# Optimization experiments

Hardware: AMD Instinct MI355X
Metric: run time of the kernel (lower is better)

Reference implementation:

```python
import jax, jax.numpy as jnp
import numpy as np

N_NODES = 100000
DIM = 4
N_EDGES = 3200000


def setup_inputs() -> dict:
    key = jax.random.key(0)
    k1, k2, k3 = jax.random.split(key, 3)
    x = jax.random.normal(k1, (N_NODES, DIM), dtype=jnp.float32)
    edge_index = jax.random.randint(k2, (2, N_EDGES), 0, N_NODES, dtype=jnp.int64)
    boo_values = jax.random.normal(k3, (N_EDGES, DIM, DIM), dtype=jnp.float32)
    return {"x": x, "edge_index": edge_index, "boo_values": boo_values}


def _spmv(x, edge_index, A):
    # y_i = sum_j A_{ij} x_j ; edge e = (row=edge_index[0], col=edge_index[1])
    # PyG flow='target_to_source': gather x at col, scatter-add at row.
    row, col = edge_index[0], edge_index[1]
    msg = jnp.einsum('eij,ej->ei', A, x[col])  # [E, dim]
    return jax.ops.segment_sum(msg, row, num_segments=x.shape[0])


def _spmv_t(x, edge_index, A):
    # y_j = sum_i A_{ij}^T x_i ; flow='source_to_target': gather at row, scatter at col.
    row, col = edge_index[0], edge_index[1]
    msg = jnp.einsum('eji,ej->ei', A, x[row])  # A^T matvec, [E, dim]
    return jax.ops.segment_sum(msg, col, num_segments=x.shape[0])


def reference(x, edge_index, boo_values):
    lt_x = _spmv_t(x, edge_index, boo_values)   # L^T x
    return _spmv(lt_x, edge_index, boo_values)  # L (L^T x)
```

## Files before the change

### kernel.cpp

```cpp
#include <hip/hip_runtime.h>

static constexpr int N_NODES = 100000;
static constexpr int N_EDGES = 3200000;
static constexpr int SHIFT  = 8;
static constexpr int NPB    = 1 << SHIFT;
static constexpr int NBK    = (N_NODES + NPB - 1) / NPB;
static constexpr int WGC    = 1024;
static constexpr int CHUNK  = N_EDGES / WGC;


__global__ void __launch_bounds__(256) k_count(
    const int* __restrict__ row, const int* __restrict__ col,
    unsigned* __restrict__ cmC, unsigned* __restrict__ cmR)
{
    __shared__ unsigned hC[NBK], hR[NBK];
    for (int b = threadIdx.x; b < NBK; b += 256) { hC[b] = 0u; hR[b] = 0u; }
    __syncthreads();
    int w = blockIdx.x, e0 = w * CHUNK;
    for (int e = e0 + threadIdx.x; e < e0 + CHUNK; e += 256) {
        atomicAdd(&hC[col[e] >> SHIFT], 1u);
        atomicAdd(&hR[row[e] >> SHIFT], 1u);
    }
    __syncthreads();
    for (int b = threadIdx.x; b < NBK; b += 256) {
        cmC[(size_t)b * WGC + w] = hC[b];
        cmR[(size_t)b * WGC + w] = hR[b];
    }
}

__global__ void __launch_bounds__(256) k_prefix(
    unsigned* __restrict__ cmC, unsigned* __restrict__ cmR,
    unsigned* __restrict__ totC, unsigned* __restrict__ totR)
{
    int warp = (blockIdx.x * 256 + threadIdx.x) >> 6;
    int lane = threadIdx.x & 63;
    if (warp >= 2 * NBK) return;
    unsigned* cm  = (warp < NBK) ? cmC : cmR;
    unsigned* tot = (warp < NBK) ? totC : totR;
    int b = (warp < NBK) ? warp : warp - NBK;
    unsigned* rowp = cm + (size_t)b * WGC;
    unsigned carry = 0;
    for (int base = 0; base < WGC; base += 64) {
        unsigned v = rowp[base + lane];
        unsigned inc = v;
        for (int off = 1; off < 64; off <<= 1) {
            unsigned t = __shfl_up(inc, off, 64);
            if (lane >= off) inc += t;
        }
        rowp[base + lane] = carry + inc - v;
        carry += __shfl(inc, 63, 64);
    }
    if (lane == 0) tot[b] = carry;
}

__global__ void __launch_bounds__(256) k_scan(
    const unsigned* __restrict__ totC, const unsigned* __restrict__ totR,
    unsigned* __restrict__ baseC, unsigned* __restrict__ baseR)
{
    const unsigned* tot = blockIdx.x ? totR : totC;
    unsigned* base = blockIdx.x ? baseR : baseC;
    __shared__ unsigned tsum[256];
    int tid = threadIdx.x;
    unsigned a0 = (2 * tid     < NBK) ? tot[2 * tid]     : 0u;
    unsigned a1 = (2 * tid + 1 < NBK) ? tot[2 * tid + 1] : 0u;
    tsum[tid] = a0 + a1;
    __syncthreads();
    for (int off = 1; off < 256; off <<= 1) {
        unsigned v = (tid >= off) ? tsum[tid - off] : 0u;
        __syncthreads();
        tsum[tid] += v;
        __syncthreads();
    }
    unsigned ex = tid ? tsum[tid - 1] : 0u;
    if (2 * tid     < NBK) base[2 * tid]     = ex;
    if (2 * tid + 1 < NBK) base[2 * tid + 1] = ex + a0;
}

__global__ void __launch_bounds__(256) k_partition(
    const int* __restrict__ key,
    const int* __restrict__ pay,
    const unsigned* __restrict__ cm,
    const unsigned* __restrict__ base,
    uint2* __restrict__ perm)
{
    __shared__ unsigned hist[NBK];
    __shared__ unsigned runstart[NBK + 1];
    __shared__ unsigned gdst[NBK];
    __shared__ unsigned tsum[256];
    __shared__ uint2 stage[CHUNK];
    int w = blockIdx.x, tid = threadIdx.x, e0 = w * CHUNK;

    for (int b = tid; b < NBK; b += 256) {
        hist[b] = 0u;
        gdst[b] = base[b] + cm[(size_t)b * WGC + w];
    }
    __syncthreads();
    for (int e = e0 + tid; e < e0 + CHUNK; e += 256)
        atomicAdd(&hist[key[e] >> SHIFT], 1u);
    __syncthreads();
    unsigned a0 = (2 * tid     < NBK) ? hist[2 * tid]     : 0u;
    unsigned a1 = (2 * tid + 1 < NBK) ? hist[2 * tid + 1] : 0u;
    tsum[tid] = a0 + a1;
    __syncthreads();
    for (int off = 1; off < 256; off <<= 1) {
        unsigned v = (tid >= off) ? tsum[tid - off] : 0u;
        __syncthreads();
        tsum[tid] += v;
        __syncthreads();
    }
    unsigned ex = tid ? tsum[tid - 1] : 0u;
    if (2 * tid     <= NBK) runstart[2 * tid]     = ex;
    if (2 * tid + 1 <= NBK) runstart[2 * tid + 1] = ex + a0;
    __syncthreads();
    for (int b = tid; b < NBK; b += 256) hist[b] = runstart[b];
    __syncthreads();
    for (int e = e0 + tid; e < e0 + CHUNK; e += 256) {
        int k = key[e], p = pay[e];
        int b = k >> SHIFT;
        unsigned pos = atomicAdd(&hist[b], 1u);
        stage[pos] = make_uint2((unsigned)e,
                                (unsigned)p | ((unsigned)(k & (NPB - 1)) << 17));
    }
    __syncthreads();
    for (int s = tid; s < CHUNK; s += 256) {
        int lo = 0, hi = NBK;
        while (hi - lo > 1) {
            int mid = (lo + hi) >> 1;
            if (runstart[mid] <= (unsigned)s) lo = mid; else hi = mid;
        }
        perm[(size_t)gdst[lo] + (unsigned)s - runstart[lo]] = stage[s];
    }
}

template<int TRANS>
__global__ void __launch_bounds__(512) k_reduce(
    const uint2* __restrict__ perm,
    const float4* __restrict__ vin,
    const float4* __restrict__ boo,
    const unsigned* __restrict__ base, const unsigned* __restrict__ tot,
    float4* __restrict__ vout)
{
    __shared__ float acc[4][NPB];
    int b = blockIdx.x, tid = threadIdx.x;
    for (int i = tid; i < 4 * NPB; i += 512) ((float*)acc)[i] = 0.f;
    __syncthreads();
    unsigned start = base[b], n = tot[b];
    for (unsigned i = start + tid; i < start + n; i += 512) {
        uint2 rec = perm[i];
        unsigned e   = rec.x;
        unsigned src = rec.y & 0x1FFFFu;
        unsigned loc = rec.y >> 17;
        float4 v  = vin[src];
        float4 a0 = boo[(size_t)e * 4 + 0];
        float4 a1 = boo[(size_t)e * 4 + 1];
        float4 a2 = boo[(size_t)e * 4 + 2];
        float4 a3 = boo[(size_t)e * 4 + 3];
        float m0, m1, m2, m3;
        if (TRANS) {
            m0 = a0.x * v.x + a1.x * v.y + a2.x * v.z + a3.x * v.w;
            m1 = a0.y * v.x + a1.y * v.y + a2.y * v.z + a3.y * v.w;
            m2 = a0.z * v.x + a1.z * v.y + a2.z * v.z + a3.z * v.w;
            m3 = a0.w * v.x + a1.w * v.y + a2.w * v.z + a3.w * v.w;
        } else {
            m0 = a0.x * v.x + a0.y * v.y + a0.z * v.z + a0.w * v.w;
            m1 = a1.x * v.x + a1.y * v.y + a1.z * v.z + a1.w * v.w;
            m2 = a2.x * v.x + a2.y * v.y + a2.z * v.z + a2.w * v.w;
            m3 = a3.x * v.x + a3.y * v.y + a3.z * v.z + a3.w * v.w;
        }
        atomicAdd(&acc[0][loc], m0);
        atomicAdd(&acc[1][loc], m1);
        atomicAdd(&acc[2][loc], m2);
        atomicAdd(&acc[3][loc], m3);
    }
    __syncthreads();
    for (int i = tid; i < NPB; i += 512) {
        int node = b * NPB + i;
        if (node < N_NODES)
            vout[node] = make_float4(acc[0][i], acc[1][i], acc[2][i], acc[3][i]);
    }
}


__global__ void __launch_bounds__(256) llt_pass1(
    const float* __restrict__ x, const int* __restrict__ row_idx,
    const int* __restrict__ col_idx, const float* __restrict__ boo,
    float* __restrict__ lt)
{
    int t = blockIdx.x * blockDim.x + threadIdx.x;
    if (t >= N_EDGES * 4) return;
    int e = t >> 2, i = t & 3;
    int r = row_idx[e], c = col_idx[e];
    const float* A = boo + (size_t)e * 16;
    const float* xv = x + (size_t)r * 4;
    float m = A[0*4+i]*xv[0] + A[1*4+i]*xv[1] + A[2*4+i]*xv[2] + A[3*4+i]*xv[3];
    atomicAdd(lt + (size_t)c * 4 + i, m);
}

__global__ void __launch_bounds__(256) llt_pass2(
    const float4* __restrict__ lt, const int* __restrict__ row_idx,
    const int* __restrict__ col_idx, const float4* __restrict__ boo,
    float* __restrict__ out)
{
    int t = blockIdx.x * blockDim.x + threadIdx.x;
    if (t >= N_EDGES * 4) return;
    int e = t >> 2, i = t & 3;
    int r = row_idx[e], c = col_idx[e];
    float4 arow = boo[(size_t)e * 4 + i];
    float4 lv = lt[c];
    float m = arow.x*lv.x + arow.y*lv.y + arow.z*lv.z + arow.w*lv.w;
    atomicAdd(out + (size_t)r * 4 + i, m);
}


extern "C" void kernel_launch(void* const* d_in, const int* in_sizes, int n_in,
                              void* d_out, int out_size, void* d_ws, size_t ws_size,
                              hipStream_t stream) {
    const float4* x = (const float4*)d_in[0];
    const int* edge_index = (const int*)d_in[1];
    const float4* boo = (const float4*)d_in[2];
    const int* row = edge_index;
    const int* col = edge_index + N_EDGES;
    float4* out = (float4*)d_out;

    auto align256 = [](size_t v) { return (v + 255) & ~(size_t)255; };
    const size_t sz_cm   = align256((size_t)NBK * WGC * 4);
    const size_t sz_vec  = align256((size_t)NBK * 4);
    const size_t sz_perm = align256((size_t)N_EDGES * 8);
    const size_t sz_lt   = align256((size_t)NBK * NPB * 16);
    const size_t need = 2 * sz_cm + 4 * sz_vec + sz_perm + sz_lt;

    if (ws_size >= need) {
        char* p = (char*)d_ws;
        unsigned* cmC   = (unsigned*)p; p += sz_cm;
        unsigned* cmR   = (unsigned*)p; p += sz_cm;
        unsigned* totC  = (unsigned*)p; p += sz_vec;
        unsigned* totR  = (unsigned*)p; p += sz_vec;
        unsigned* baseC = (unsigned*)p; p += sz_vec;
        unsigned* baseR = (unsigned*)p; p += sz_vec;
        uint2*    perm  = (uint2*)p;    p += sz_perm;
        float4*   lt    = (float4*)p;   p += sz_lt;

        k_count<<<WGC, 256, 0, stream>>>(row, col, cmC, cmR);
        k_prefix<<<(2 * NBK + 3) / 4, 256, 0, stream>>>(cmC, cmR, totC, totR);
        k_scan<<<2, 256, 0, stream>>>(totC, totR, baseC, baseR);
        k_partition<<<WGC, 256, 0, stream>>>(col, row, cmC, baseC, perm);
        k_reduce<1><<<NBK, 512, 0, stream>>>(perm, x, boo, baseC, totC, lt);
        k_partition<<<WGC, 256, 0, stream>>>(row, col, cmR, baseR, perm);
        k_reduce<0><<<NBK, 512, 0, stream>>>(perm, (const float4*)lt, boo, baseR, totR, out);
    } else {
        float* ltf = (float*)d_ws;
        hipMemsetAsync(ltf, 0, (size_t)N_NODES * 4 * sizeof(float), stream);
        hipMemsetAsync(out, 0, (size_t)N_NODES * 4 * sizeof(float), stream);
        const int grid = (N_EDGES * 4 + 255) / 256;
        llt_pass1<<<grid, 256, 0, stream>>>((const float*)x, row, col, (const float*)boo, ltf);
        llt_pass2<<<grid, 256, 0, stream>>>((const float4*)ltf, row, col, boo, (float*)out);
    }
}
```

Measured before the change: 265.4 us.

## Compute messages in partition pass, scatter bf16-packed messages with byte tags

The per-edge 4x4 matvec moves from the reduce kernel into the partition kernel. There the boo values are read in edge order (coalesced) rather than through a permuted gather. The resulting message is packed into four bf16 values (8 bytes) plus a one-byte local-node tag and scattered into bucket order, so the reduce kernel only streams messages and does LDS atomics. The work-group count also rises from 1024 to 1280. Rounding messages to bf16 adds precision loss in both passes, which could exceed tolerance.

```diff
diff --git a/kernel.cpp b/kernel.cpp
--- a/kernel.cpp
+++ b/kernel.cpp
@@ -5,9 +5,17 @@
 static constexpr int SHIFT  = 8;
 static constexpr int NPB    = 1 << SHIFT;
 static constexpr int NBK    = (N_NODES + NPB - 1) / NPB;
-static constexpr int WGC    = 1024;
+static constexpr int WGC    = 1280;
 static constexpr int CHUNK  = N_EDGES / WGC;
 
+__device__ __forceinline__ unsigned bf16rne(float f) {
+    unsigned u = __float_as_uint(f);
+    u += 0x7fffu + ((u >> 16) & 1u);
+    return u >> 16;
+}
+__device__ __forceinline__ unsigned pack2(float lo, float hi) {
+    return bf16rne(lo) | (bf16rne(hi) << 16);
+}
 
 __global__ void __launch_bounds__(256) k_count(
     const int* __restrict__ row, const int* __restrict__ col,
@@ -76,18 +84,23 @@
     if (2 * tid + 1 < NBK) base[2 * tid + 1] = ex + a0;
 }
 
-__global__ void __launch_bounds__(256) k_partition(
+template<int TRANS>
+__global__ void __launch_bounds__(256) k_partition_msg(
     const int* __restrict__ key,
     const int* __restrict__ pay,
+    const float4* __restrict__ vin,
+    const float4* __restrict__ boo,
     const unsigned* __restrict__ cm,
     const unsigned* __restrict__ base,
-    uint2* __restrict__ perm)
-{
+    uint2* __restrict__ msgbuf, unsigned char* __restrict__ tagbuf)
+{
+    __shared__ int      karr[CHUNK];
+    __shared__ uint2    smsg[CHUNK];
+    __shared__ unsigned char stag[CHUNK];
     __shared__ unsigned hist[NBK];
     __shared__ unsigned runstart[NBK + 1];
     __shared__ unsigned gdst[NBK];
     __shared__ unsigned tsum[256];
-    __shared__ uint2 stage[CHUNK];
     int w = blockIdx.x, tid = threadIdx.x, e0 = w * CHUNK;
 
     for (int b = tid; b < NBK; b += 256) {
@@ -95,8 +108,11 @@
         gdst[b] = base[b] + cm[(size_t)b * WGC + w];
     }
     __syncthreads();
-    for (int e = e0 + tid; e < e0 + CHUNK; e += 256)
-        atomicAdd(&hist[key[e] >> SHIFT], 1u);
+    for (int l = tid; l < CHUNK; l += 256) {
+        int k = key[e0 + l];
+        karr[l] = k;
+        atomicAdd(&hist[k >> SHIFT], 1u);
+    }
     __syncthreads();
     unsigned a0 = (2 * tid     < NBK) ? hist[2 * tid]     : 0u;
     unsigned a1 = (2 * tid + 1 < NBK) ? hist[2 * tid + 1] : 0u;
@@ -114,29 +130,49 @@
     __syncthreads();
     for (int b = tid; b < NBK; b += 256) hist[b] = runstart[b];
     __syncthreads();
-    for (int e = e0 + tid; e < e0 + CHUNK; e += 256) {
-        int k = key[e], p = pay[e];
+
+    for (int l = tid; l < CHUNK; l += 256) {
+        int e = e0 + l;
+        int k = karr[l];
+        int p = pay[e];
         int b = k >> SHIFT;
+        float4 v  = vin[p];
+        float4 q0 = boo[(size_t)e * 4 + 0];
+        float4 q1 = boo[(size_t)e * 4 + 1];
+        float4 q2 = boo[(size_t)e * 4 + 2];
+        float4 q3 = boo[(size_t)e * 4 + 3];
+        float m0, m1, m2, m3;
+        if (TRANS) {
+            m0 = q0.x * v.x + q1.x * v.y + q2.x * v.z + q3.x * v.w;
+            m1 = q0.y * v.x + q1.y * v.y + q2.y * v.z + q3.y * v.w;
+            m2 = q0.z * v.x + q1.z * v.y + q2.z * v.z + q3.z * v.w;
+            m3 = q0.w * v.x + q1.w * v.y + q2.w * v.z + q3.w * v.w;
+        } else {
+            m0 = q0.x * v.x + q0.y * v.y + q0.z * v.z + q0.w * v.w;
+            m1 = q1.x * v.x + q1.y * v.y + q1.z * v.z + q1.w * v.w;
+            m2 = q2.x * v.x + q2.y * v.y + q2.z * v.z + q2.w * v.w;
+            m3 = q3.x * v.x + q3.y * v.y + q3.z * v.z + q3.w * v.w;
+        }
         unsigned pos = atomicAdd(&hist[b], 1u);
-        stage[pos] = make_uint2((unsigned)e,
-                                (unsigned)p | ((unsigned)(k & (NPB - 1)) << 17));
-    }
-    __syncthreads();
+        smsg[pos] = make_uint2(pack2(m0, m1), pack2(m2, m3));
+        stag[pos] = (unsigned char)(k & (NPB - 1));
+    }
+    __syncthreads();
+
     for (int s = tid; s < CHUNK; s += 256) {
         int lo = 0, hi = NBK;
         while (hi - lo > 1) {
             int mid = (lo + hi) >> 1;
             if (runstart[mid] <= (unsigned)s) lo = mid; else hi = mid;
         }
-        perm[(size_t)gdst[lo] + (unsigned)s - runstart[lo]] = stage[s];
-    }
-}
-
-template<int TRANS>
-__global__ void __launch_bounds__(512) k_reduce(
-    const uint2* __restrict__ perm,
-    const float4* __restrict__ vin,
-    const float4* __restrict__ boo,
+        size_t g = (size_t)gdst[lo] + (unsigned)s - runstart[lo];
+        msgbuf[g] = smsg[s];
+        tagbuf[g] = stag[s];
+    }
+}
+
+__global__ void __launch_bounds__(512) k_reduce_msg(
+    const uint2* __restrict__ msgbuf, const unsigned char* __restrict__ tagbuf,
     const unsigned* __restrict__ base, const unsigned* __restrict__ tot,
     float4* __restrict__ vout)
 {
@@ -146,31 +182,12 @@
     __syncthreads();
     unsigned start = base[b], n = tot[b];
     for (unsigned i = start + tid; i < start + n; i += 512) {
-        uint2 rec = perm[i];
-        unsigned e   = rec.x;
-        unsigned src = rec.y & 0x1FFFFu;
-        unsigned loc = rec.y >> 17;
-        float4 v  = vin[src];
-        float4 a0 = boo[(size_t)e * 4 + 0];
-        float4 a1 = boo[(size_t)e * 4 + 1];
-        float4 a2 = boo[(size_t)e * 4 + 2];
-        float4 a3 = boo[(size_t)e * 4 + 3];
-        float m0, m1, m2, m3;
-        if (TRANS) {
-            m0 = a0.x * v.x + a1.x * v.y + a2.x * v.z + a3.x * v.w;
-            m1 = a0.y * v.x + a1.y * v.y + a2.y * v.z + a3.y * v.w;
-            m2 = a0.z * v.x + a1.z * v.y + a2.z * v.z + a3.z * v.w;
-            m3 = a0.w * v.x + a1.w * v.y + a2.w * v.z + a3.w * v.w;
-        } else {
-            m0 = a0.x * v.x + a0.y * v.y + a0.z * v.z + a0.w * v.w;
-            m1 = a1.x * v.x + a1.y * v.y + a1.z * v.z + a1.w * v.w;
-            m2 = a2.x * v.x + a2.y * v.y + a2.z * v.z + a2.w * v.w;
-            m3 = a3.x * v.x + a3.y * v.y + a3.z * v.z + a3.w * v.w;
-        }
-        atomicAdd(&acc[0][loc], m0);
-        atomicAdd(&acc[1][loc], m1);
-        atomicAdd(&acc[2][loc], m2);
-        atomicAdd(&acc[3][loc], m3);
+        uint2 m = msgbuf[i];
+        int loc = tagbuf[i];
+        atomicAdd(&acc[0][loc], __uint_as_float(m.x << 16));
+        atomicAdd(&acc[1][loc], __uint_as_float(m.x & 0xffff0000u));
+        atomicAdd(&acc[2][loc], __uint_as_float(m.y << 16));
+        atomicAdd(&acc[3][loc], __uint_as_float(m.y & 0xffff0000u));
     }
     __syncthreads();
     for (int i = tid; i < NPB; i += 512) {
@@ -225,9 +242,10 @@
     auto align256 = [](size_t v) { return (v + 255) & ~(size_t)255; };
     const size_t sz_cm   = align256((size_t)NBK * WGC * 4);
     const size_t sz_vec  = align256((size_t)NBK * 4);
-    const size_t sz_perm = align256((size_t)N_EDGES * 8);
+    const size_t sz_msg  = align256((size_t)N_EDGES * 8);
+    const size_t sz_tag  = align256((size_t)N_EDGES);
     const size_t sz_lt   = align256((size_t)NBK * NPB * 16);
-    const size_t need = 2 * sz_cm + 4 * sz_vec + sz_perm + sz_lt;
+    const size_t need = 2 * sz_cm + 4 * sz_vec + sz_msg + sz_tag + sz_lt;
 
     if (ws_size >= need) {
         char* p = (char*)d_ws;
@@ -237,16 +255,17 @@
         unsigned* totR  = (unsigned*)p; p += sz_vec;
         unsigned* baseC = (unsigned*)p; p += sz_vec;
         unsigned* baseR = (unsigned*)p; p += sz_vec;
-        uint2*    perm  = (uint2*)p;    p += sz_perm;
+        uint2*    msg   = (uint2*)p;    p += sz_msg;
+        unsigned char* tag = (unsigned char*)p; p += sz_tag;
         float4*   lt    = (float4*)p;   p += sz_lt;
 
         k_count<<<WGC, 256, 0, stream>>>(row, col, cmC, cmR);
         k_prefix<<<(2 * NBK + 3) / 4, 256, 0, stream>>>(cmC, cmR, totC, totR);
         k_scan<<<2, 256, 0, stream>>>(totC, totR, baseC, baseR);
-        k_partition<<<WGC, 256, 0, stream>>>(col, row, cmC, baseC, perm);
-        k_reduce<1><<<NBK, 512, 0, stream>>>(perm, x, boo, baseC, totC, lt);
-        k_partition<<<WGC, 256, 0, stream>>>(row, col, cmR, baseR, perm);
-        k_reduce<0><<<NBK, 512, 0, stream>>>(perm, (const float4*)lt, boo, baseR, totR, out);
+        k_partition_msg<1><<<WGC, 256, 0, stream>>>(col, row, x, boo, cmC, baseC, msg, tag);
+        k_reduce_msg<<<NBK, 512, 0, stream>>>(msg, tag, baseC, totC, lt);
+        k_partition_msg<0><<<WGC, 256, 0, stream>>>(row, col, (const float4*)lt, boo, cmR, baseR, msg, tag);
+        k_reduce_msg<<<NBK, 512, 0, stream>>>(msg, tag, baseR, totR, out);
     } else {
         float* ltf = (float*)d_ws;
         hipMemsetAsync(ltf, 0, (size_t)N_NODES * 4 * sizeof(float), stream);
```

Result: slower. 398.4 us (+50.1%).

## Split reduce blocks four ways with lane-per-row edge processing and merge pass

Applied to the files above, without the earlier changes.

Each bucket's reduce is now split across four workgroups, with the partial sums written to separate buffers and combined by a new merge kernel. Inside the reduce, four lanes share one edge and each loads one row of the 4x4 block, which gives coalesced 64-byte loads. The transposed case reduces its products across those lanes with shuffles. The aim is more parallelism (391 blocks become 1564) and better memory coalescing, at the cost of extra partial-buffer traffic, two extra launches, and redundant loads of perm and vin per lane.

```diff
diff --git a/kernel.cpp b/kernel.cpp
--- a/kernel.cpp
+++ b/kernel.cpp
@@ -5,8 +5,10 @@
 static constexpr int SHIFT  = 8;
 static constexpr int NPB    = 1 << SHIFT;
 static constexpr int NBK    = (N_NODES + NPB - 1) / NPB;
+static constexpr int SLOTS  = NBK * NPB;
 static constexpr int WGC    = 1024;
 static constexpr int CHUNK  = N_EDGES / WGC;
+static constexpr int PSPLIT = 4;
 
 
 __global__ void __launch_bounds__(256) k_count(
@@ -138,46 +140,55 @@
     const float4* __restrict__ vin,
     const float4* __restrict__ boo,
     const unsigned* __restrict__ base, const unsigned* __restrict__ tot,
-    float4* __restrict__ vout)
-{
-    __shared__ float acc[4][NPB];
-    int b = blockIdx.x, tid = threadIdx.x;
-    for (int i = tid; i < 4 * NPB; i += 512) ((float*)acc)[i] = 0.f;
+    float4* __restrict__ part)
+{
+    __shared__ float acc[NPB][4];
+    int b = blockIdx.x / PSPLIT, sub = blockIdx.x % PSPLIT;
+    int tid = threadIdx.x;
+    for (int i = tid; i < NPB * 4; i += 512) ((float*)acc)[i] = 0.f;
     __syncthreads();
     unsigned start = base[b], n = tot[b];
-    for (unsigned i = start + tid; i < start + n; i += 512) {
+    int g = tid >> 2;
+    int q = tid & 3;
+    for (unsigned i = start + sub * 128 + g; i < start + n; i += 128 * PSPLIT) {
         uint2 rec = perm[i];
         unsigned e   = rec.x;
         unsigned src = rec.y & 0x1FFFFu;
         unsigned loc = rec.y >> 17;
         float4 v  = vin[src];
-        float4 a0 = boo[(size_t)e * 4 + 0];
-        float4 a1 = boo[(size_t)e * 4 + 1];
-        float4 a2 = boo[(size_t)e * 4 + 2];
-        float4 a3 = boo[(size_t)e * 4 + 3];
-        float m0, m1, m2, m3;
+        float4 ch = boo[(size_t)e * 4 + q];
+        float mq;
         if (TRANS) {
-            m0 = a0.x * v.x + a1.x * v.y + a2.x * v.z + a3.x * v.w;
-            m1 = a0.y * v.x + a1.y * v.y + a2.y * v.z + a3.y * v.w;
-            m2 = a0.z * v.x + a1.z * v.y + a2.z * v.z + a3.z * v.w;
-            m3 = a0.w * v.x + a1.w * v.y + a2.w * v.z + a3.w * v.w;
+            float vq = (q == 0) ? v.x : (q == 1) ? v.y : (q == 2) ? v.z : v.w;
+            float p0 = vq * ch.x, p1 = vq * ch.y, p2 = vq * ch.z, p3 = vq * ch.w;
+            p0 += __shfl_xor(p0, 1); p1 += __shfl_xor(p1, 1);
+            p2 += __shfl_xor(p2, 1); p3 += __shfl_xor(p3, 1);
+            p0 += __shfl_xor(p0, 2); p1 += __shfl_xor(p1, 2);
+            p2 += __shfl_xor(p2, 2); p3 += __shfl_xor(p3, 2);
+            mq = (q == 0) ? p0 : (q == 1) ? p1 : (q == 2) ? p2 : p3;
         } else {
-            m0 = a0.x * v.x + a0.y * v.y + a0.z * v.z + a0.w * v.w;
-            m1 = a1.x * v.x + a1.y * v.y + a1.z * v.z + a1.w * v.w;
-            m2 = a2.x * v.x + a2.y * v.y + a2.z * v.z + a2.w * v.w;
-            m3 = a3.x * v.x + a3.y * v.y + a3.z * v.z + a3.w * v.w;
+            mq = ch.x * v.x + ch.y * v.y + ch.z * v.z + ch.w * v.w;
         }
-        atomicAdd(&acc[0][loc], m0);
-        atomicAdd(&acc[1][loc], m1);
-        atomicAdd(&acc[2][loc], m2);
-        atomicAdd(&acc[3][loc], m3);
+        atomicAdd(&acc[loc][q], mq);
     }
     __syncthreads();
     for (int i = tid; i < NPB; i += 512) {
-        int node = b * NPB + i;
-        if (node < N_NODES)
-            vout[node] = make_float4(acc[0][i], acc[1][i], acc[2][i], acc[3][i]);
-    }
+        part[(size_t)sub * SLOTS + (size_t)b * NPB + i] =
+            make_float4(acc[i][0], acc[i][1], acc[i][2], acc[i][3]);
+    }
+}
+
+__global__ void __launch_bounds__(256) k_merge(
+    const float4* __restrict__ part, float4* __restrict__ vout)
+{
+    int s = blockIdx.x * 256 + threadIdx.x;
+    if (s >= N_NODES) return;
+    float4 r = part[s];
+    for (int sub = 1; sub < PSPLIT; ++sub) {
+        float4 t = part[(size_t)sub * SLOTS + s];
+        r.x += t.x; r.y += t.y; r.z += t.z; r.w += t.w;
+    }
+    vout[s] = r;
 }
 
 
@@ -226,8 +237,9 @@
     const size_t sz_cm   = align256((size_t)NBK * WGC * 4);
     const size_t sz_vec  = align256((size_t)NBK * 4);
     const size_t sz_perm = align256((size_t)N_EDGES * 8);
-    const size_t sz_lt   = align256((size_t)NBK * NPB * 16);
-    const size_t need = 2 * sz_cm + 4 * sz_vec + sz_perm + sz_lt;
+    const size_t sz_lt   = align256((size_t)SLOTS * 16);
+    const size_t sz_part = align256((size_t)PSPLIT * SLOTS * 16);
+    const size_t need = 2 * sz_cm + 4 * sz_vec + sz_perm + sz_lt + sz_part;
 
     if (ws_size >= need) {
         char* p = (char*)d_ws;
@@ -239,14 +251,17 @@
         unsigned* baseR = (unsigned*)p; p += sz_vec;
         uint2*    perm  = (uint2*)p;    p += sz_perm;
         float4*   lt    = (float4*)p;   p += sz_lt;
+        float4*   part  = (float4*)p;   p += sz_part;
 
         k_count<<<WGC, 256, 0, stream>>>(row, col, cmC, cmR);
         k_prefix<<<(2 * NBK + 3) / 4, 256, 0, stream>>>(cmC, cmR, totC, totR);
         k_scan<<<2, 256, 0, stream>>>(totC, totR, baseC, baseR);
         k_partition<<<WGC, 256, 0, stream>>>(col, row, cmC, baseC, perm);
-        k_reduce<1><<<NBK, 512, 0, stream>>>(perm, x, boo, baseC, totC, lt);
+        k_reduce<1><<<NBK * PSPLIT, 512, 0, stream>>>(perm, x, boo, baseC, totC, part);
+        k_merge<<<(N_NODES + 255) / 256, 256, 0, stream>>>(part, lt);
         k_partition<<<WGC, 256, 0, stream>>>(row, col, cmR, baseR, perm);
-        k_reduce<0><<<NBK, 512, 0, stream>>>(perm, (const float4*)lt, boo, baseR, totR, out);
+        k_reduce<0><<<NBK * PSPLIT, 512, 0, stream>>>(perm, (const float4*)lt, boo, baseR, totR, part);
+        k_merge<<<(N_NODES + 255) / 256, 256, 0, stream>>>(part, out);
     } else {
         float* ltf = (float*)d_ws;
         hipMemsetAsync(ltf, 0, (size_t)N_NODES * 4 * sizeof(float), stream);
```

Result: no change. 262.5 us (-1.1%).

## Use coarse node buckets with split reduction blocks and partial-sum merge

Applied to the files above, without the earlier changes.

Replaces the 391 power-of-two node buckets with 26 buckets of 3848 nodes each. This cuts per-block histogram, scan and counter-matrix work in the count, prefix and partition kernels, and the shared scans become serial loops. Each bucket's reduction is split across 20 workgroups, each writing a private partial-sum slice, and a new merge kernel sums the 20 slices. The cost is extra global traffic for partial buffers, two more launches, and more shared memory per reduce block, which may lower occupancy.

```diff
diff --git a/kernel.cpp b/kernel.cpp
--- a/kernel.cpp
+++ b/kernel.cpp
@@ -2,11 +2,12 @@
 
 static constexpr int N_NODES = 100000;
 static constexpr int N_EDGES = 3200000;
-static constexpr int SHIFT  = 8;
-static constexpr int NPB    = 1 << SHIFT;
-static constexpr int NBK    = (N_NODES + NPB - 1) / NPB;
+static constexpr int NBK    = 26;
+static constexpr int NPB    = 3848;
+static constexpr int SLOTS  = NBK * NPB;
 static constexpr int WGC    = 1024;
 static constexpr int CHUNK  = N_EDGES / WGC;
+static constexpr int PSPLIT = 20;
 
 
 __global__ void __launch_bounds__(256) k_count(
@@ -14,17 +15,17 @@
     unsigned* __restrict__ cmC, unsigned* __restrict__ cmR)
 {
     __shared__ unsigned hC[NBK], hR[NBK];
-    for (int b = threadIdx.x; b < NBK; b += 256) { hC[b] = 0u; hR[b] = 0u; }
+    if (threadIdx.x < NBK) { hC[threadIdx.x] = 0u; hR[threadIdx.x] = 0u; }
     __syncthreads();
     int w = blockIdx.x, e0 = w * CHUNK;
     for (int e = e0 + threadIdx.x; e < e0 + CHUNK; e += 256) {
-        atomicAdd(&hC[col[e] >> SHIFT], 1u);
-        atomicAdd(&hR[row[e] >> SHIFT], 1u);
-    }
-    __syncthreads();
-    for (int b = threadIdx.x; b < NBK; b += 256) {
-        cmC[(size_t)b * WGC + w] = hC[b];
-        cmR[(size_t)b * WGC + w] = hR[b];
+        atomicAdd(&hC[col[e] / NPB], 1u);
+        atomicAdd(&hR[row[e] / NPB], 1u);
+    }
+    __syncthreads();
+    if (threadIdx.x < NBK) {
+        cmC[(size_t)threadIdx.x * WGC + w] = hC[threadIdx.x];
+        cmR[(size_t)threadIdx.x * WGC + w] = hR[threadIdx.x];
     }
 }
 
@@ -53,73 +54,55 @@
     if (lane == 0) tot[b] = carry;
 }
 
-__global__ void __launch_bounds__(256) k_scan(
+__global__ void __launch_bounds__(64) k_scan(
     const unsigned* __restrict__ totC, const unsigned* __restrict__ totR,
     unsigned* __restrict__ baseC, unsigned* __restrict__ baseR)
 {
-    const unsigned* tot = blockIdx.x ? totR : totC;
-    unsigned* base = blockIdx.x ? baseR : baseC;
-    __shared__ unsigned tsum[256];
-    int tid = threadIdx.x;
-    unsigned a0 = (2 * tid     < NBK) ? tot[2 * tid]     : 0u;
-    unsigned a1 = (2 * tid + 1 < NBK) ? tot[2 * tid + 1] : 0u;
-    tsum[tid] = a0 + a1;
-    __syncthreads();
-    for (int off = 1; off < 256; off <<= 1) {
-        unsigned v = (tid >= off) ? tsum[tid - off] : 0u;
-        __syncthreads();
-        tsum[tid] += v;
-        __syncthreads();
-    }
-    unsigned ex = tid ? tsum[tid - 1] : 0u;
-    if (2 * tid     < NBK) base[2 * tid]     = ex;
-    if (2 * tid + 1 < NBK) base[2 * tid + 1] = ex + a0;
-}
-
-__global__ void __launch_bounds__(256) k_partition(
+    if (threadIdx.x == 0) {
+        unsigned s = 0;
+        for (int b = 0; b < NBK; ++b) { baseC[b] = s; s += totC[b]; }
+    } else if (threadIdx.x == 1) {
+        unsigned s = 0;
+        for (int b = 0; b < NBK; ++b) { baseR[b] = s; s += totR[b]; }
+    }
+}
+
+__global__ void __launch_bounds__(256) k_part(
     const int* __restrict__ key,
     const int* __restrict__ pay,
     const unsigned* __restrict__ cm,
     const unsigned* __restrict__ base,
     uint2* __restrict__ perm)
 {
+    __shared__ uint2 stage[CHUNK];
     __shared__ unsigned hist[NBK];
     __shared__ unsigned runstart[NBK + 1];
     __shared__ unsigned gdst[NBK];
-    __shared__ unsigned tsum[256];
-    __shared__ uint2 stage[CHUNK];
     int w = blockIdx.x, tid = threadIdx.x, e0 = w * CHUNK;
 
-    for (int b = tid; b < NBK; b += 256) {
-        hist[b] = 0u;
-        gdst[b] = base[b] + cm[(size_t)b * WGC + w];
+    if (tid < NBK) {
+        hist[tid] = 0u;
+        gdst[tid] = base[tid] + cm[(size_t)tid * WGC + w];
     }
     __syncthreads();
     for (int e = e0 + tid; e < e0 + CHUNK; e += 256)
-        atomicAdd(&hist[key[e] >> SHIFT], 1u);
-    __syncthreads();
-    unsigned a0 = (2 * tid     < NBK) ? hist[2 * tid]     : 0u;
-    unsigned a1 = (2 * tid + 1 < NBK) ? hist[2 * tid + 1] : 0u;
-    tsum[tid] = a0 + a1;
-    __syncthreads();
-    for (int off = 1; off < 256; off <<= 1) {
-        unsigned v = (tid >= off) ? tsum[tid - off] : 0u;
-        __syncthreads();
-        tsum[tid] += v;
-        __syncthreads();
-    }
-    unsigned ex = tid ? tsum[tid - 1] : 0u;
-    if (2 * tid     <= NBK) runstart[2 * tid]     = ex;
-    if (2 * tid + 1 <= NBK) runstart[2 * tid + 1] = ex + a0;
-    __syncthreads();
-    for (int b = tid; b < NBK; b += 256) hist[b] = runstart[b];
+        atomicAdd(&hist[key[e] / NPB], 1u);
+    __syncthreads();
+    if (tid == 0) {
+        unsigned s = 0;
+        for (int b = 0; b < NBK; ++b) { runstart[b] = s; s += hist[b]; }
+        runstart[NBK] = s;
+    }
+    __syncthreads();
+    if (tid < NBK) hist[tid] = runstart[tid];
     __syncthreads();
     for (int e = e0 + tid; e < e0 + CHUNK; e += 256) {
         int k = key[e], p = pay[e];
-        int b = k >> SHIFT;
+        int b = k / NPB;
+        int loc = k - b * NPB;
         unsigned pos = atomicAdd(&hist[b], 1u);
         stage[pos] = make_uint2((unsigned)e,
-                                (unsigned)p | ((unsigned)(k & (NPB - 1)) << 17));
+                                (unsigned)p | ((unsigned)loc << 17));
     }
     __syncthreads();
     for (int s = tid; s < CHUNK; s += 256) {
@@ -138,14 +121,17 @@
     const float4* __restrict__ vin,
     const float4* __restrict__ boo,
     const unsigned* __restrict__ base, const unsigned* __restrict__ tot,
-    float4* __restrict__ vout)
+    float4* __restrict__ part)
 {
     __shared__ float acc[4][NPB];
-    int b = blockIdx.x, tid = threadIdx.x;
+    int b = blockIdx.x / PSPLIT, sub = blockIdx.x % PSPLIT;
+    int tid = threadIdx.x;
     for (int i = tid; i < 4 * NPB; i += 512) ((float*)acc)[i] = 0.f;
     __syncthreads();
     unsigned start = base[b], n = tot[b];
-    for (unsigned i = start + tid; i < start + n; i += 512) {
+    unsigned lo = start + (unsigned)(((unsigned long long)n * sub) / PSPLIT);
+    unsigned hi = start + (unsigned)(((unsigned long long)n * (sub + 1)) / PSPLIT);
+    for (unsigned i = lo + tid; i < hi; i += 512) {
         uint2 rec = perm[i];
         unsigned e   = rec.x;
         unsigned src = rec.y & 0x1FFFFu;
@@ -173,11 +159,22 @@
         atomicAdd(&acc[3][loc], m3);
     }
     __syncthreads();
-    for (int i = tid; i < NPB; i += 512) {
-        int node = b * NPB + i;
-        if (node < N_NODES)
-            vout[node] = make_float4(acc[0][i], acc[1][i], acc[2][i], acc[3][i]);
-    }
+    float4* dst = part + (size_t)sub * SLOTS + (size_t)b * NPB;
+    for (int i = tid; i < NPB; i += 512)
+        dst[i] = make_float4(acc[0][i], acc[1][i], acc[2][i], acc[3][i]);
+}
+
+__global__ void __launch_bounds__(256) k_merge(
+    const float4* __restrict__ part, float4* __restrict__ vout)
+{
+    int s = blockIdx.x * 256 + threadIdx.x;
+    if (s >= N_NODES) return;
+    float4 r = part[s];
+    for (int sub = 1; sub < PSPLIT; ++sub) {
+        float4 t = part[(size_t)sub * SLOTS + s];
+        r.x += t.x; r.y += t.y; r.z += t.z; r.w += t.w;
+    }
+    vout[s] = r;
 }
 
 
@@ -226,8 +223,9 @@
     const size_t sz_cm   = align256((size_t)NBK * WGC * 4);
     const size_t sz_vec  = align256((size_t)NBK * 4);
     const size_t sz_perm = align256((size_t)N_EDGES * 8);
-    const size_t sz_lt   = align256((size_t)NBK * NPB * 16);
-    const size_t need = 2 * sz_cm + 4 * sz_vec + sz_perm + sz_lt;
+    const size_t sz_lt   = align256((size_t)N_NODES * 16);
+    const size_t sz_part = align256((size_t)PSPLIT * SLOTS * 16);
+    const size_t need = 2 * sz_cm + 4 * sz_vec + sz_perm + sz_lt + sz_part;
 
     if (ws_size >= need) {
         char* p = (char*)d_ws;
@@ -239,14 +237,17 @@
         unsigned* baseR = (unsigned*)p; p += sz_vec;
         uint2*    perm  = (uint2*)p;    p += sz_perm;
         float4*   lt    = (float4*)p;   p += sz_lt;
+        float4*   part  = (float4*)p;   p += sz_part;
 
         k_count<<<WGC, 256, 0, stream>>>(row, col, cmC, cmR);
-        k_prefix<<<(2 * NBK + 3) / 4, 256, 0, stream>>>(cmC, cmR, totC, totR);
-        k_scan<<<2, 256, 0, stream>>>(totC, totR, baseC, baseR);
-        k_partition<<<WGC, 256, 0, stream>>>(col, row, cmC, baseC, perm);
-        k_reduce<1><<<NBK, 512, 0, stream>>>(perm, x, boo, baseC, totC, lt);
-        k_partition<<<WGC, 256, 0, stream>>>(row, col, cmR, baseR, perm);
-        k_reduce<0><<<NBK, 512, 0, stream>>>(perm, (const float4*)lt, boo, baseR, totR, out);
+        k_prefix<<<(2 * NBK * 64 + 255) / 256, 256, 0, stream>>>(cmC, cmR, totC, totR);
+        k_scan<<<1, 64, 0, stream>>>(totC, totR, baseC, baseR);
+        k_part<<<WGC, 256, 0, stream>>>(col, row, cmC, baseC, perm);
+        k_reduce<1><<<NBK * PSPLIT, 512, 0, stream>>>(perm, x, boo, baseC, totC, part);
+        k_merge<<<(N_NODES + 255) / 256, 256, 0, stream>>>(part, lt);
+        k_part<<<WGC, 256, 0, stream>>>(row, col, cmR, baseR, perm);
+        k_reduce<0><<<NBK * PSPLIT, 512, 0, stream>>>(perm, (const float4*)lt, boo, baseR, totR, part);
+        k_merge<<<(N_NODES + 255) / 256, 256, 0, stream>>>(part, out);
     } else {
         float* ltf = (float*)d_ws;
         hipMemsetAsync(ltf, 0, (size_t)N_NODES * 4 * sizeof(float), stream);
```

New measurement: 282.1 us. 1.06x slower.
